# Kernel optimization log

Measured on AMD Instinct MI355X. Metric: run time of the kernel, lower is better.

## Reference

```python
import jax, jax.numpy as jnp
import numpy as np

INNER_LR = 0.001
INNER_STEPS = 3
EPS = 1e-8


def setup_inputs() -> dict:
    key = jax.random.key(0)
    ks = jax.random.split(key, 9)
    B_, H, K = 16384, 512, 64
    return {
        "R_U": jax.random.normal(ks[0], (B_, H, 3), dtype=jnp.float32),
        "alpha": jax.random.uniform(ks[1], (B_,), dtype=jnp.float32),
        "beta": jax.random.uniform(ks[2], (B_,), dtype=jnp.float32),
        "lambdas": jax.random.uniform(ks[3], (3,), dtype=jnp.float32),
        "B": jax.random.normal(ks[4], (H, K), dtype=jnp.float32),
        "B_dot": jax.random.normal(ks[5], (H, K), dtype=jnp.float32),
        "B_ddot": jax.random.normal(ks[6], (H, K), dtype=jnp.float32),
        "B_dddot": jax.random.normal(ks[7], (H, K), dtype=jnp.float32),
        "B_pinv": jax.random.normal(ks[8], (K, H), dtype=jnp.float32),
    }


def _inner_opt(R_U, alpha, beta, lambdas, B, B_dot, B_ddot, B_dddot, B_pinv):
    l1, l2, l3 = lambdas[0], lambdas[1], lambdas[2]

    def per_sample(r, a, b):
        # r: (H,3); C: (K,3)
        C0 = B_pinv @ r

        def loss_fn(C):
            P = B @ C            # (H,3)
            V = B_dot @ C        # (H,3)
            A = B_ddot @ C       # (H,3)
            J = B_dddot @ C      # (H,3)
            v_norm_raw = jnp.linalg.norm(V, axis=-1)          # (H,) used in power-law loss
            v_norm_eps = v_norm_raw + EPS                      # used in curvature (torch adds eps)
            cross = jnp.cross(V, A)                            # (H,3)
            kappa = jnp.linalg.norm(cross, axis=-1) / (v_norm_eps ** 3 + EPS)
            pos_loss = jnp.sum((P - r) ** 2, axis=-1)          # (H,)
            kappa_safe = jnp.clip(kappa, 1e-4, 1e4)
            log_power = jnp.clip(b * jnp.log(kappa_safe), -10.0, 10.0)
            target = jnp.clip(a * jnp.exp(log_power), 1e-6, 1e6)
            power_law_loss = (v_norm_raw - target) ** 2        # (H,)
            jerk_loss = jnp.sum(J ** 2, axis=-1)               # (H,)
            return jnp.sum(l1 * pos_loss + l2 * power_law_loss + l3 * jerk_loss)

        def step(C, _):
            g = jax.grad(loss_fn)(C)
            return C - INNER_LR * g, None

        C, _ = jax.lax.scan(step, C0, None, length=INNER_STEPS)
        return C

    return jax.vmap(per_sample)(R_U, alpha, beta)  # (batch, K, 3)


def reference(R_U, alpha, beta, lambdas, B, B_dot, B_ddot, B_dddot, B_pinv):
    return _inner_opt(R_U, alpha, beta, lambdas, B, B_dot, B_ddot, B_dddot, B_pinv)
```

## Files before the change

kernel.cpp:

```cpp
#include <hip/hip_runtime.h>
#include <math.h>

#define EPSF 1e-8f
#define LR   1e-3f

#define HH 512
#define KK 64
#define SS 4
#define PbStr 36
#define GbStr 136
#define SLICE 4096
#define PbOff 0
#define GbOff 1792

typedef short    bf16x8 __attribute__((ext_vector_type(8)));
typedef _Float16 f16x8  __attribute__((ext_vector_type(8)));
typedef float    f32x4  __attribute__((ext_vector_type(4)));

__device__ __forceinline__ unsigned short f2bf(float x) {
  unsigned int u = __float_as_uint(x);
  return (unsigned short)((u + 0x7fffu + ((u >> 16) & 1u)) >> 16);
}
__device__ __forceinline__ float bfhi(float x) {
  return __uint_as_float(((unsigned int)f2bf(x)) << 16);
}
__device__ __forceinline__ unsigned short f2h(float x) {
  _Float16 h = (_Float16)x;
  return *(unsigned short*)&h;
}

__global__ void prep_kernel(const float* __restrict__ B,
                            const float* __restrict__ Bd,
                            const float* __restrict__ Bdd,
                            const float* __restrict__ Bddd,
                            const float* __restrict__ Bp,
                            unsigned short* __restrict__ ws) {
  int tid = blockIdx.x * 256 + threadIdx.x;
  const float* Ms[4] = {B, Bd, Bdd, Bddd};
  unsigned short bits[2];
  if (tid < 65536) {
    #pragma unroll
    for (int t = 0; t < 2; ++t) {
      unsigned int id = 2u * tid + t;
      int j = id & 7, lane = (id >> 3) & 63;
      int mt = (id >> 9) & 3, ks2 = (id >> 11) & 3;
      int qtr = (id >> 13) & 3, chunk = (id >> 15) & 3;
      int khat = mt * 16 + (lane & 15);
      int kq = ((lane >> 4) << 3) + j;
      int h = chunk * 128 + qtr * 32 + kq;
      bits[t] = f2bf(Ms[ks2][h * 64 + khat]);
    }
    ((unsigned int*)ws)[tid] = ((unsigned int)bits[1] << 16) | bits[0];
  } else if (tid < 131072) {
    int base = tid - 65536;
    #pragma unroll
    for (int t = 0; t < 2; ++t) {
      unsigned int id = 2u * base + t;
      int j = id & 7, lane = (id >> 3) & 63, kap = (id >> 9) & 1;
      int ht = (id >> 10) & 31, z = (id >> 15) & 3;
      int h = ht * 16 + (lane & 15);
      int kk = kap * 32 + ((lane >> 4) << 3) + j;
      bits[t] = f2h(Ms[z][h * 64 + kk]);
    }
    ((unsigned int*)(ws + 131072))[base] = ((unsigned int)bits[1] << 16) | bits[0];
  } else {
    int base = tid - 131072;
    #pragma unroll
    for (int t = 0; t < 2; ++t) {
      unsigned int id = 2u * base + t;
      int j = id & 7, lane = (id >> 3) & 63, hilo = (id >> 9) & 1;
      int mt = (id >> 10) & 3, ks = (id >> 12) & 15;
      int khat = mt * 16 + (lane & 15);
      int Kl = ks * 32 + ((lane >> 4) << 3) + j;
      float val = Bp[khat * 512 + Kl];
      float hi = bfhi(val);
      bits[t] = hilo ? f2bf(val - hi) : f2bf(hi);
    }
    ((unsigned int*)(ws + 262144))[base] = ((unsigned int)bits[1] << 16) | bits[0];
  }
}

__global__ __launch_bounds__(256, 4)
void copt_kernel(const float* __restrict__ R_U,
                 const float* __restrict__ alpha,
                 const float* __restrict__ beta,
                 const float* __restrict__ lambdas,
                 const unsigned short* __restrict__ ws,
                 float* __restrict__ out) {
  __shared__ __align__(16) float Cl[SS][KK][4];
  __shared__ __align__(16) unsigned short Cbf[2 * 512];
  __shared__ __align__(16) unsigned short pool[4 * SLICE];

  const unsigned short* AFb = ws;
  const unsigned short* AFf = ws + 131072;
  const unsigned short* AFp = ws + 262144;

  const int tid  = threadIdx.x;
  const int lane = tid & 63;
  const int wid  = tid >> 6;
  const int quad = lane >> 4;
  const int c    = lane & 15;

  const float l1 = lambdas[0], l2 = lambdas[1], l3 = lambdas[2];
  const int bg = blockIdx.x * SS;

  if (tid < 512) ((unsigned int*)Cbf)[tid] = 0u;

  {
    const int s = wid, sg = bg + s;
    const float4* rp = (const float4*)(R_U + (size_t)sg * (HH * 3));
    #pragma unroll
    for (int i = 0; i < 6; ++i) {
      float4 v = rp[i * 64 + lane];
      int e = (i * 64 + lane) * 4;
      const float* pv = &v.x;
      #pragma unroll
      for (int d = 0; d < 4; ++d) {
        int ee = e + d, h = ee / 3, m = ee - 3 * h;
        pool[(3 * s + m) * 520 + h] = f2bf(pv[d]);
      }
    }
  }
  __syncthreads();

  {
    f32x4 cacc = {0.f, 0.f, 0.f, 0.f};
    const unsigned short* gb = &pool[c * 520 + quad * 8];
    #pragma unroll 4
    for (int ks = 0; ks < 16; ++ks) {
      const unsigned short* pA = AFp + (size_t)((ks * 4 + wid) * 2) * 512 + lane * 8;
      bf16x8 ah = *(const bf16x8*)pA;
      bf16x8 al = *(const bf16x8*)(pA + 512);
      bf16x8 gg = *(const bf16x8*)(gb + ks * 32);
      cacc = __builtin_amdgcn_mfma_f32_16x16x32_bf16(ah, gg, cacc, 0, 0, 0);
      cacc = __builtin_amdgcn_mfma_f32_16x16x32_bf16(al, gg, cacc, 0, 0, 0);
    }
    if (c < 12) {
      const int s = (c * 86) >> 8, m = c - 3 * s;
      const int kr = wid * 16 + quad * 4;
      #pragma unroll
      for (int r = 0; r < 4; ++r) {
        float val = cacc[r];
        int k = kr + r;
        Cl[s][k][m] = val;
        Cbf[(k >> 5) * 512 + (((k >> 3) & 3) * 16 + c) * 8 + (k & 7)] = f2h(val);
      }
    }
  }
  __syncthreads();

  const int hq = lane & 31;
  const int es0 = 2 * (lane >> 5), es1 = es0 + 1;
  const float ea0 = alpha[bg + es0], ea1 = alpha[bg + es1];
  const float eb0 = beta[bg + es0],  eb1 = beta[bg + es1];
  const float* er0 = R_U + (size_t)(bg + es0) * (HH * 3);
  const float* er1 = R_U + (size_t)(bg + es1) * (HH * 3);

  unsigned short* Pb = pool + wid * SLICE + PbOff;
  unsigned short* Gb = pool + wid * SLICE + GbOff;

  auto elem = [&](const float acc[12], float aa, float bb,
                  const float* rp, float g[12]) {
    float P0=acc[0],P1=acc[1],P2=acc[2];
    float V0=acc[3],V1=acc[4],V2=acc[5];
    float A0=acc[6],A1=acc[7],A2=acc[8];
    float J0=acc[9],J1=acc[10],J2=acc[11];
    float v2 = V0*V0 + V1*V1 + V2*V2;
    float v  = __builtin_amdgcn_sqrtf(v2);
    float ve = v + EPSF;
    float cx0 = V1*A2 - V2*A1;
    float cx1 = V2*A0 - V0*A2;
    float cx2 = V0*A1 - V1*A0;
    float nc  = __builtin_amdgcn_sqrtf(cx0*cx0 + cx1*cx1 + cx2*cx2);
    float ve2 = ve*ve;
    float denom = ve2*ve + EPSF;
    float invd  = __builtin_amdgcn_rcpf(denom);
    float kappa = nc * invd;
    float ks  = fminf(fmaxf(kappa, 1e-4f), 1e4f);
    float lpr = bb * __logf(ks);
    float lp  = fminf(fmaxf(lpr, -10.f), 10.f);
    float tr  = aa * __expf(lp);
    float tt  = fminf(fmaxf(tr, 1e-6f), 1e6f);
    float s2  = 2.f*l2*(v - tt);
    float gtr  = (tr > 1e-6f && tr < 1e6f) ? -s2 : 0.f;
    float glpr = (lpr > -10.f && lpr < 10.f) ? gtr*tr : 0.f;
    float gk   = (kappa > 1e-4f && kappa < 1e4f)
                   ? glpr*bb*__builtin_amdgcn_rcpf(ks) : 0.f;
    float gnc  = gk * invd;
    float gden = -gk * kappa * invd;
    float gve  = 3.f * ve2 * gden;
    float gv   = s2 + gve;
    float giv  = gv * __builtin_amdgcn_rcpf(v);
    float gcs  = gnc * __builtin_amdgcn_rcpf(nc);
    float gc0 = gcs*cx0, gc1 = gcs*cx1, gc2 = gcs*cx2;
    g[0]  = 2.f*l1*(P0 - rp[0]);
    g[1]  = 2.f*l1*(P1 - rp[1]);
    g[2]  = 2.f*l1*(P2 - rp[2]);
    g[3]  = fmaf(giv, V0, A1*gc2 - A2*gc1);
    g[4]  = fmaf(giv, V1, A2*gc0 - A0*gc2);
    g[5]  = fmaf(giv, V2, A0*gc1 - A1*gc0);
    g[6]  = gc1*V2 - gc2*V1;
    g[7]  = gc2*V0 - gc0*V2;
    g[8]  = gc0*V1 - gc1*V0;
    g[9]  = 2.f*l3*J0;
    g[10] = 2.f*l3*J1;
    g[11] = 2.f*l3*J2;
  };

  for (int it = 0; it < 3; ++it) {
    f32x4 gacc[4];
    #pragma unroll
    for (int mt = 0; mt < 4; ++mt) gacc[mt] = (f32x4){0.f, 0.f, 0.f, 0.f};

    f16x8 cf0 = *(const f16x8*)&Cbf[lane * 8];
    f16x8 cf1 = *(const f16x8*)&Cbf[512 + lane * 8];

    for (int q = 0; q < 4; ++q) {
      #pragma unroll
      for (int ht = 0; ht < 2; ++ht) {
        const int htg = wid * 8 + q * 2 + ht;
        #pragma unroll
        for (int z = 0; z < 4; ++z) {
          const unsigned short* pA =
              AFf + (size_t)((z * 32 + htg) * 2) * 512 + lane * 8;
          f16x8 af0 = *(const f16x8*)pA;
          f16x8 af1 = *(const f16x8*)(pA + 512);
          f32x4 d = {0.f, 0.f, 0.f, 0.f};
          d = __builtin_amdgcn_mfma_f32_16x16x32_f16(af0, cf0, d, 0, 0, 0);
          d = __builtin_amdgcn_mfma_f32_16x16x32_f16(af1, cf1, d, 0, 0, 0);
          if (c < 12) {
            uint2 pk;
            pk.x = (unsigned int)f2h(d[0]) | ((unsigned int)f2h(d[1]) << 16);
            pk.y = (unsigned int)f2h(d[2]) | ((unsigned int)f2h(d[3]) << 16);
            *(uint2*)&Pb[(z * 12 + c) * PbStr + ht * 16 + quad * 4] = pk;
          }
        }
      }

      {
        float acc0[12], acc1[12];
        #pragma unroll
        for (int z = 0; z < 4; ++z)
          #pragma unroll
          for (int m = 0; m < 3; ++m) {
            acc0[z*3+m] = (float)*(const _Float16*)&Pb[(z*12 + 3*es0 + m) * PbStr + hq];
            acc1[z*3+m] = (float)*(const _Float16*)&Pb[(z*12 + 3*es1 + m) * PbStr + hq];
          }
        const int hg = wid * 128 + q * 32 + hq;
        float g0[12], g1[12];
        elem(acc0, ea0, eb0, er0 + (size_t)hg * 3, g0);
        elem(acc1, ea1, eb1, er1 + (size_t)hg * 3, g1);
        #pragma unroll
        for (int z = 0; z < 4; ++z)
          #pragma unroll
          for (int m = 0; m < 3; ++m) {
            Gb[(3*es0 + m) * GbStr + z*32 + hq] = f2bf(g0[z*3 + m]);
            Gb[(3*es1 + m) * GbStr + z*32 + hq] = f2bf(g1[z*3 + m]);
          }
      }

      #pragma unroll
      for (int ks2 = 0; ks2 < 4; ++ks2) {
        bf16x8 gg = *(const bf16x8*)&Gb[c * GbStr + ks2 * 32 + quad * 8];
        #pragma unroll
        for (int mt = 0; mt < 4; ++mt) {
          const unsigned short* pA =
              AFb + (size_t)(((wid * 4 + q) * 4 + ks2) * 4 + mt) * 512 + lane * 8;
          bf16x8 a = *(const bf16x8*)pA;
          gacc[mt] = __builtin_amdgcn_mfma_f32_16x16x32_bf16(a, gg, gacc[mt], 0, 0, 0);
        }
      }
    }

    {
      char* poolB = (char*)pool;
      #pragma unroll
      for (int mt = 0; mt < 4; ++mt)
        *(f32x4*)(poolB + wid * 8192 + mt * 1024 + lane * 16) = gacc[mt];
    }
    __syncthreads();
    {
      const char* poolB = (const char*)pool;
      f32x4 tot = {0.f, 0.f, 0.f, 0.f};
      #pragma unroll
      for (int v = 0; v < 4; ++v)
        tot += *(const f32x4*)(poolB + v * 8192 + wid * 1024 + lane * 16);
      if (c < 12) {
        const int s = (c * 86) >> 8, m = c - 3 * s;
        const int kr = wid * 16 + quad * 4;
        #pragma unroll
        for (int r = 0; r < 4; ++r) {
          int k = kr + r;
          float val = Cl[s][k][m] - LR * tot[r];
          Cl[s][k][m] = val;
          Cbf[(k >> 5) * 512 + (((k >> 3) & 3) * 16 + c) * 8 + (k & 7)] = f2h(val);
        }
      }
    }
    __syncthreads();
  }

  const int ps = wid, psg = bg + ps;
  float* op = out + ((size_t)psg * KK + lane) * 3;
  op[0] = Cl[ps][lane][0];
  op[1] = Cl[ps][lane][1];
  op[2] = Cl[ps][lane][2];
}

extern "C" void kernel_launch(void* const* d_in, const int* in_sizes, int n_in,
                              void* d_out, int out_size, void* d_ws, size_t ws_size,
                              hipStream_t stream) {
  const float* R_U     = (const float*)d_in[0];
  const float* alpha   = (const float*)d_in[1];
  const float* beta    = (const float*)d_in[2];
  const float* lambdas = (const float*)d_in[3];
  const float* B       = (const float*)d_in[4];
  const float* Bd      = (const float*)d_in[5];
  const float* Bdd     = (const float*)d_in[6];
  const float* Bddd    = (const float*)d_in[7];
  const float* Bp      = (const float*)d_in[8];
  unsigned short* ws = (unsigned short*)d_ws;
  const int nB = in_sizes[1];

  hipLaunchKernelGGL(prep_kernel, dim3(640), dim3(256), 0, stream,
                     B, Bd, Bdd, Bddd, Bp, ws);
  hipLaunchKernelGGL(copt_kernel, dim3(nB / SS), dim3(256), 0, stream,
                     R_U, alpha, beta, lambdas, ws, (float*)d_out);
}
```

Baseline: 411.6 us.

## Shrink LDS footprint and overlap P/G buffers to raise occupancy

Reduces per-wave LDS slice size by aliasing the projection and gradient staging buffers and trimming the C storage padding, and raises the launch-bounds occupancy target from 4 to 7 blocks. The projection tile is transposed so each thread reads its 12 values with vectorized half4 loads instead of scalar strided reads, and gradient bf16 conversion uses a packed conversion intrinsic. This aims to increase waves per CU and cut LDS instruction count, but the tighter launch bound may force register spills, and overlapping buffers relies on ordering within a wave.

```diff
diff --git a/kernel.cpp b/kernel.cpp
--- a/kernel.cpp
+++ b/kernel.cpp
@@ -1,4 +1,5 @@
 #include <hip/hip_runtime.h>
+#include <hip/hip_bf16.h>
 #include <math.h>
 
 #define EPSF 1e-8f
@@ -7,14 +8,13 @@
 #define HH 512
 #define KK 64
 #define SS 4
-#define PbStr 36
+#define PbStr 56
 #define GbStr 136
-#define SLICE 4096
-#define PbOff 0
-#define GbOff 1792
+#define SLICE 2176
 
 typedef short    bf16x8 __attribute__((ext_vector_type(8)));
 typedef _Float16 f16x8  __attribute__((ext_vector_type(8)));
+typedef _Float16 f16x4  __attribute__((ext_vector_type(4)));
 typedef float    f32x4  __attribute__((ext_vector_type(4)));
 
 __device__ __forceinline__ unsigned short f2bf(float x) {
@@ -27,6 +27,11 @@
 __device__ __forceinline__ unsigned short f2h(float x) {
   _Float16 h = (_Float16)x;
   return *(unsigned short*)&h;
+}
+__device__ __forceinline__ unsigned int pkbf2(float a, float b) {
+  union { __hip_bfloat162 h; unsigned int u; } cv;
+  cv.h = __float22bfloat162_rn(make_float2(a, b));
+  return cv.u;
 }
 
 __global__ void prep_kernel(const float* __restrict__ B,
@@ -80,14 +85,14 @@
   }
 }
 
-__global__ __launch_bounds__(256, 4)
+__global__ __launch_bounds__(256, 7)
 void copt_kernel(const float* __restrict__ R_U,
                  const float* __restrict__ alpha,
                  const float* __restrict__ beta,
                  const float* __restrict__ lambdas,
                  const unsigned short* __restrict__ ws,
                  float* __restrict__ out) {
-  __shared__ __align__(16) float Cl[SS][KK][4];
+  __shared__ __align__(16) float Cl[SS][KK][3];
   __shared__ __align__(16) unsigned short Cbf[2 * 512];
   __shared__ __align__(16) unsigned short pool[4 * SLICE];
 
@@ -156,8 +161,10 @@
   const float* er0 = R_U + (size_t)(bg + es0) * (HH * 3);
   const float* er1 = R_U + (size_t)(bg + es1) * (HH * 3);
 
-  unsigned short* Pb = pool + wid * SLICE + PbOff;
-  unsigned short* Gb = pool + wid * SLICE + GbOff;
+  unsigned short* Pbh = pool + wid * SLICE;
+  unsigned short* Gbu = pool + wid * SLICE;
+
+  const int fs = (c * 86) >> 8, fm = c - 3 * fs;
 
   auto elem = [&](const float acc[12], float aa, float bb,
                   const float* rp, float g[12]) {
@@ -229,23 +236,32 @@
           d = __builtin_amdgcn_mfma_f32_16x16x32_f16(af0, cf0, d, 0, 0, 0);
           d = __builtin_amdgcn_mfma_f32_16x16x32_f16(af1, cf1, d, 0, 0, 0);
           if (c < 12) {
-            uint2 pk;
-            pk.x = (unsigned int)f2h(d[0]) | ((unsigned int)f2h(d[1]) << 16);
-            pk.y = (unsigned int)f2h(d[2]) | ((unsigned int)f2h(d[3]) << 16);
-            *(uint2*)&Pb[(z * 12 + c) * PbStr + ht * 16 + quad * 4] = pk;
+            unsigned short* pp =
+                Pbh + (ht * 16 + quad * 4) * PbStr + fs * 12 + z * 3 + fm;
+            pp[0 * PbStr] = f2h(d[0]);
+            pp[1 * PbStr] = f2h(d[1]);
+            pp[2 * PbStr] = f2h(d[2]);
+            pp[3 * PbStr] = f2h(d[3]);
           }
         }
       }
 
       {
+        const unsigned short* p0 = Pbh + hq * PbStr + es0 * 12;
+        const unsigned short* p1 = Pbh + hq * PbStr + es1 * 12;
+        f16x4 a0 = *(const f16x4*)(p0);
+        f16x4 a1 = *(const f16x4*)(p0 + 4);
+        f16x4 a2 = *(const f16x4*)(p0 + 8);
+        f16x4 b0v = *(const f16x4*)(p1);
+        f16x4 b1v = *(const f16x4*)(p1 + 4);
+        f16x4 b2v = *(const f16x4*)(p1 + 8);
         float acc0[12], acc1[12];
         #pragma unroll
-        for (int z = 0; z < 4; ++z)
-          #pragma unroll
-          for (int m = 0; m < 3; ++m) {
-            acc0[z*3+m] = (float)*(const _Float16*)&Pb[(z*12 + 3*es0 + m) * PbStr + hq];
-            acc1[z*3+m] = (float)*(const _Float16*)&Pb[(z*12 + 3*es1 + m) * PbStr + hq];
-          }
+        for (int j = 0; j < 4; ++j) {
+          acc0[j]     = (float)a0[j];  acc1[j]     = (float)b0v[j];
+          acc0[4 + j] = (float)a1[j];  acc1[4 + j] = (float)b1v[j];
+          acc0[8 + j] = (float)a2[j];  acc1[8 + j] = (float)b2v[j];
+        }
         const int hg = wid * 128 + q * 32 + hq;
         float g0[12], g1[12];
         elem(acc0, ea0, eb0, er0 + (size_t)hg * 3, g0);
@@ -254,14 +270,15 @@
         for (int z = 0; z < 4; ++z)
           #pragma unroll
           for (int m = 0; m < 3; ++m) {
-            Gb[(3*es0 + m) * GbStr + z*32 + hq] = f2bf(g0[z*3 + m]);
-            Gb[(3*es1 + m) * GbStr + z*32 + hq] = f2bf(g1[z*3 + m]);
+            unsigned int pk = pkbf2(g0[z*3 + m], g1[z*3 + m]);
+            Gbu[(3*es0 + m) * GbStr + z*32 + hq] = (unsigned short)pk;
+            Gbu[(3*es1 + m) * GbStr + z*32 + hq] = (unsigned short)(pk >> 16);
           }
       }
 
       #pragma unroll
       for (int ks2 = 0; ks2 < 4; ++ks2) {
-        bf16x8 gg = *(const bf16x8*)&Gb[c * GbStr + ks2 * 32 + quad * 8];
+        bf16x8 gg = *(const bf16x8*)&Gbu[c * GbStr + ks2 * 32 + quad * 8];
         #pragma unroll
         for (int mt = 0; mt < 4; ++mt) {
           const unsigned short* pA =
@@ -273,18 +290,18 @@
     }
 
     {
-      char* poolB = (char*)pool;
+      float* dmp = (float*)pool + wid * (SLICE / 2);
       #pragma unroll
       for (int mt = 0; mt < 4; ++mt)
-        *(f32x4*)(poolB + wid * 8192 + mt * 1024 + lane * 16) = gacc[mt];
+        *(f32x4*)(dmp + mt * 256 + lane * 4) = gacc[mt];
     }
     __syncthreads();
     {
-      const char* poolB = (const char*)pool;
+      const float* poolF = (const float*)pool;
       f32x4 tot = {0.f, 0.f, 0.f, 0.f};
       #pragma unroll
       for (int v = 0; v < 4; ++v)
-        tot += *(const f32x4*)(poolB + v * 8192 + wid * 1024 + lane * 16);
+        tot += *(const f32x4*)(poolF + v * (SLICE / 2) + wid * 256 + lane * 4);
       if (c < 12) {
         const int s = (c * 86) >> 8, m = c - 3 * s;
         const int kr = wid * 16 + quad * 4;
```

Result: slower. 740.5 us (+79.9%).
